# Kernel tuning notes

Measured on AMD Instinct MI355X. Metric: run time of the kernel, lower is better.

Reference implementation:

```python
import jax, jax.numpy as jnp
import numpy as np

N_NODES = 100000
N_EDGES = 1600000
IN_CH = 128
HID = 128   # 2 * out_channels
OUT_CH = 64


def setup_inputs() -> dict:
    key = jax.random.key(0)
    k1, k2, k3, k4, k5, k6 = jax.random.split(key, 6)
    x = jax.random.normal(k1, (N_NODES, IN_CH), dtype=jnp.float32)
    edge_index = jax.random.randint(k2, (2, N_EDGES), 0, N_NODES, dtype=jnp.int64)
    W1 = jax.random.normal(k3, (IN_CH, HID), dtype=jnp.float32) / np.sqrt(IN_CH)
    b1 = jax.random.normal(k4, (HID,), dtype=jnp.float32) * 0.01
    W2 = jax.random.normal(k5, (HID, OUT_CH), dtype=jnp.float32) / np.sqrt(HID)
    b2 = jax.random.normal(k6, (OUT_CH,), dtype=jnp.float32) * 0.01
    return {"x": x, "edge_index": edge_index, "W1": W1, "b1": b1, "W2": W2, "b2": b2}


def _gcn_layer(x, src, dst, norm, W, b, n_nodes):
    # GCNConv: linear transform, then normalized scatter-add aggregation + bias
    h = x @ W                                   # [N, d_out]
    msg = h[src] * norm[:, None]                # gather + edge normalize, [E+N, d_out]
    out = jax.ops.segment_sum(msg, dst, num_segments=n_nodes)
    return out + b


def reference(x, edge_index, W1, b1, W2, b2):
    n = x.shape[0]
    loop = jnp.arange(n, dtype=edge_index.dtype)
    # add self-loops (PyG GCNConv default)
    src = jnp.concatenate([edge_index[0], loop])
    dst = jnp.concatenate([edge_index[1], loop])
    # symmetric normalization deg^-1/2[src] * deg^-1/2[dst]
    deg = jax.ops.segment_sum(jnp.ones_like(dst, x.dtype), dst, num_segments=n)
    dinv = jnp.where(deg > 0, jax.lax.rsqrt(deg), 0.0)
    norm = dinv[src] * dinv[dst]

    h = jax.nn.relu(_gcn_layer(x, src, dst, norm, W1, b1, n))
    out = jax.nn.relu(_gcn_layer(h, src, dst, norm, W2, b2, n))
    return out
```

## Files before the change

### kernel.cpp

```cpp
#include <hip/hip_runtime.h>
#include <hip/hip_fp16.h>

typedef _Float16 f16x8 __attribute__((ext_vector_type(8)));
typedef float f32x4 __attribute__((ext_vector_type(4)));

#define BSH 9
#define BSZ 512
#define CAP 12288

__global__ __launch_bounds__(256) void passA(const int* __restrict__ ei,
                                             int* __restrict__ bcount, int E, int NB) {
  __shared__ int hist[256];
  int t = threadIdx.x;
  hist[t] = 0;
  __syncthreads();
  for (int e = blockIdx.x * 256 + t; e < E; e += gridDim.x * 256)
    atomicAdd(&hist[ei[E + e] >> BSH], 1);
  __syncthreads();
  if (t < NB && hist[t]) atomicAdd(&bcount[t], hist[t]);
}

__global__ __launch_bounds__(256) void scanB(const int* __restrict__ bcount,
                                             int* __restrict__ bstart,
                                             int* __restrict__ bfill, int NB, int E) {
  __shared__ int s[256];
  int t = threadIdx.x;
  int v = (t < NB) ? bcount[t] : 0;
  s[t] = v;
  __syncthreads();
  for (int off = 1; off < 256; off <<= 1) {
    int add = (t >= off) ? s[t - off] : 0;
    __syncthreads();
    s[t] += add;
    __syncthreads();
  }
  if (t < NB) {
    int ex = s[t] - v;
    bstart[t] = ex;
    bfill[t] = ex;
  }
  if (t == 0) bstart[NB] = E;
}

template <int NC, int NWC, bool IN_F16, bool SCALE>
__device__ __forceinline__ void gemm_mfma_body(
    const void* __restrict__ Xv, const float* __restrict__ W,
    const float* __restrict__ dinv, _Float16* __restrict__ G, int nrows, int bid,
    _Float16* Bs) {
  int t = threadIdx.x;
  {
    int n = t % NC;
    int kh = (t / NC) * (NC / 2);
    constexpr int NBLK = (NC / 2) / 8;
#pragma unroll
    for (int b = 0; b < NBLK; ++b) {
      f16x8 tmp;
#pragma unroll
      for (int j = 0; j < 8; ++j)
        tmp[j] = (_Float16)W[(size_t)(kh + b * 8 + j) * NC + n];
      *(f16x8*)(&Bs[n * 136 + kh + b * 8]) = tmp;
    }
  }
  __syncthreads();

  int w = t >> 6, lane = t & 63;
  int m = lane & 15, q = lane >> 4;
  int wr = (w / NWC) * 64, wc = (w % NWC) * 64;
  int row0 = bid * ((4 / NWC) * 64);

  f32x4 acc[4][4];
#pragma unroll
  for (int rt = 0; rt < 4; ++rt)
#pragma unroll
    for (int ct = 0; ct < 4; ++ct)
#pragma unroll
      for (int qq = 0; qq < 4; ++qq) acc[rt][ct][qq] = 0.f;

#pragma unroll
  for (int kc = 0; kc < 4; ++kc) {
    int kbase = kc * 32 + q * 8;
    f16x8 af[4];
#pragma unroll
    for (int rt = 0; rt < 4; ++rt) {
      int row = row0 + wr + rt * 16 + m;
      if constexpr (IN_F16) {
        f16x8 a = {0, 0, 0, 0, 0, 0, 0, 0};
        if (row < nrows) a = *(const f16x8*)((const _Float16*)Xv + (size_t)row * 128 + kbase);
        af[rt] = a;
      } else {
        float4 x0 = {0, 0, 0, 0}, x1 = {0, 0, 0, 0};
        if (row < nrows) {
          const float* Xf = (const float*)Xv;
          x0 = *(const float4*)(Xf + (size_t)row * 128 + kbase);
          x1 = *(const float4*)(Xf + (size_t)row * 128 + kbase + 4);
        }
        f16x8 a;
        a[0] = (_Float16)x0.x; a[1] = (_Float16)x0.y;
        a[2] = (_Float16)x0.z; a[3] = (_Float16)x0.w;
        a[4] = (_Float16)x1.x; a[5] = (_Float16)x1.y;
        a[6] = (_Float16)x1.z; a[7] = (_Float16)x1.w;
        af[rt] = a;
      }
    }
    f16x8 bf[4];
#pragma unroll
    for (int ct = 0; ct < 4; ++ct) {
      int n = wc + ct * 16 + m;
      bf[ct] = *(f16x8*)(&Bs[n * 136 + kbase]);
    }
#pragma unroll
    for (int rt = 0; rt < 4; ++rt)
#pragma unroll
      for (int ct = 0; ct < 4; ++ct)
        acc[rt][ct] = __builtin_amdgcn_mfma_f32_16x16x32_f16(af[rt], bf[ct],
                                                             acc[rt][ct], 0, 0, 0);
  }
#pragma unroll
  for (int rt = 0; rt < 4; ++rt) {
#pragma unroll
    for (int r = 0; r < 4; ++r) {
      int row = row0 + wr + rt * 16 + q * 4 + r;
      if (row < nrows) {
        float d = SCALE ? dinv[row] : 1.f;
#pragma unroll
        for (int ct = 0; ct < 4; ++ct) {
          int col = wc + ct * 16 + m;
          G[(size_t)row * NC + col] = (_Float16)(acc[rt][ct][r] * d);
        }
      }
    }
  }
}

__global__ __launch_bounds__(256) void fused_gemm_passB(
    const float* __restrict__ X, const float* __restrict__ W1,
    _Float16* __restrict__ G, int nrows, int GB,
    const int* __restrict__ ei, int* __restrict__ bfill,
    unsigned int* __restrict__ pairs, int E, int PB) {
  __shared__ char smem[128 * 136 * 2];
  int g = blockIdx.x;
  int M2 = 2 * (GB < PB ? GB : PB);
  bool is_gemm;
  int bid;
  if (g < M2) { is_gemm = (g & 1) == 0; bid = g >> 1; }
  else        { is_gemm = (GB > PB);    bid = g - M2 + (GB < PB ? GB : PB); }
  if (is_gemm) {
    gemm_mfma_body<128, 2, false, false>(X, W1, nullptr, G, nrows, bid,
                                         (_Float16*)smem);
  } else {
    int* hist = (int*)smem;
    int* gbase = (int*)(smem + 1024);
    int t = threadIdx.x;
    hist[t] = 0;
    __syncthreads();
    int d[8], s[8], lp[8], bb[8];
    int base = bid * 2048;
#pragma unroll
    for (int u = 0; u < 8; ++u) {
      int e = base + u * 256 + t;
      if (e < E) {
        d[u] = ei[E + e];
        s[u] = ei[e];
        bb[u] = d[u] >> BSH;
        lp[u] = atomicAdd(&hist[bb[u]], 1);
      } else {
        bb[u] = -1;
      }
    }
    __syncthreads();
    if (hist[t]) gbase[t] = atomicAdd(&bfill[t], hist[t]);
    __syncthreads();
#pragma unroll
    for (int u = 0; u < 8; ++u)
      if (bb[u] >= 0)
        pairs[gbase[bb[u]] + lp[u]] =
            ((unsigned int)(d[u] & (BSZ - 1)) << 17) | (unsigned int)s[u];
  }
}

__global__ __launch_bounds__(512) void passC(const unsigned int* __restrict__ pairs,
                                             const int* __restrict__ bstart,
                                             int* __restrict__ rowstart,
                                             int* __restrict__ deg,
                                             float* __restrict__ dinv,
                                             int* __restrict__ csr, int N) {
  __shared__ int hcnt[BSZ];
  __shared__ int lfill[BSZ];
  __shared__ int ss[512];
  __shared__ int lcsr[CAP];
  int b = blockIdx.x;
  int t = threadIdx.x;
  int lo = bstart[b], hi = bstart[b + 1];
  int cnt = hi - lo;
  int nbase = b << BSH;
  hcnt[t] = 0;
  __syncthreads();
  for (int k = lo + t; k < hi; k += 512)
    atomicAdd(&hcnt[(pairs[k] >> 17) & (BSZ - 1)], 1);
  __syncthreads();
  int v = hcnt[t];
  ss[t] = v;
  __syncthreads();
  for (int off = 1; off < 512; off <<= 1) {
    int add = (t >= off) ? ss[t - off] : 0;
    __syncthreads();
    ss[t] += add;
    __syncthreads();
  }
  int ex = ss[t] - v;
  lfill[t] = ex;
  int node = nbase + t;
  if (node < N) {
    rowstart[node] = lo + ex;
    deg[node] = v;
    dinv[node] = rsqrtf((float)(v + 1));
  }
  __syncthreads();
  bool fits = (cnt <= CAP);
  for (int k = lo + t; k < hi; k += 512) {
    unsigned int p = pairs[k];
    int pos = atomicAdd(&lfill[(p >> 17) & (BSZ - 1)], 1);
    int src = (int)(p & 0x1FFFFu);
    if (fits) lcsr[pos] = src;
    else      csr[lo + pos] = src;
  }
  __syncthreads();
  if (fits)
    for (int k = t; k < cnt; k += 512) csr[lo + k] = lcsr[k];
}

#define HPAD 144
__global__ __launch_bounds__(256) void agg128_mm(
    const __half* __restrict__ G, const int* __restrict__ csr,
    const int* __restrict__ rowstart, const int* __restrict__ deg,
    const float* __restrict__ dinv, const float* __restrict__ b1,
    const float* __restrict__ W2, _Float16* __restrict__ g2, int N) {
  __shared__ _Float16 Ws[64 * 136];
  __shared__ _Float16 Hs[4][16 * HPAD];
  int t = threadIdx.x;
  {
    int n = t & 63;
    int kh = (t >> 6) * 32;
#pragma unroll
    for (int b = 0; b < 4; ++b) {
      f16x8 tmp;
#pragma unroll
      for (int j = 0; j < 8; ++j)
        tmp[j] = (_Float16)W2[(size_t)(kh + b * 8 + j) * 64 + n];
      *(f16x8*)(&Ws[n * 136 + kh + b * 8]) = tmp;
    }
  }
  __syncthreads();

  int w = t >> 6, lane = t & 63;
  int m = lane & 15, q = lane >> 4;
  const __half2* Gp = (const __half2*)G;
  float2 bb = ((const float2*)b1)[lane];
  int node0 = (blockIdx.x * 4 + w) * 16;
  if (node0 >= N) return;

  _Float16* H = Hs[w];
#pragma unroll 1
  for (int u = 0; u < 16; ++u) {
    int i = node0 + u;
    float2 h = {0.f, 0.f};
    if (i < N) {
      int ii = __builtin_amdgcn_readfirstlane(i);
      float di = dinv[ii];
      float2 g = __half22float2(Gp[(size_t)ii * 64 + lane]);
      float2 a = {di * g.x, di * g.y};
      int s = rowstart[ii];
      int d = deg[ii];
      int k = 0;
      for (; k + 3 < d; k += 4) {
        int s0 = csr[s + k], s1 = csr[s + k + 1];
        int s2 = csr[s + k + 2], s3 = csr[s + k + 3];
        float w0 = dinv[s0], w1 = dinv[s1], w2 = dinv[s2], w3 = dinv[s3];
        float2 v0 = __half22float2(Gp[(size_t)s0 * 64 + lane]);
        float2 v1 = __half22float2(Gp[(size_t)s1 * 64 + lane]);
        float2 v2 = __half22float2(Gp[(size_t)s2 * 64 + lane]);
        float2 v3 = __half22float2(Gp[(size_t)s3 * 64 + lane]);
        a.x = fmaf(w0, v0.x, a.x); a.y = fmaf(w0, v0.y, a.y);
        a.x = fmaf(w1, v1.x, a.x); a.y = fmaf(w1, v1.y, a.y);
        a.x = fmaf(w2, v2.x, a.x); a.y = fmaf(w2, v2.y, a.y);
        a.x = fmaf(w3, v3.x, a.x); a.y = fmaf(w3, v3.y, a.y);
      }
      for (; k < d; ++k) {
        int s0 = csr[s + k];
        float w0 = dinv[s0];
        float2 v0 = __half22float2(Gp[(size_t)s0 * 64 + lane]);
        a.x = fmaf(w0, v0.x, a.x); a.y = fmaf(w0, v0.y, a.y);
      }
      h.x = fmaxf(fmaf(di, a.x, bb.x), 0.f);
      h.y = fmaxf(fmaf(di, a.y, bb.y), 0.f);
    }
    H[u * HPAD + 2 * lane]     = (_Float16)h.x;
    H[u * HPAD + 2 * lane + 1] = (_Float16)h.y;
  }

  f32x4 acc[4];
#pragma unroll
  for (int ct = 0; ct < 4; ++ct)
#pragma unroll
    for (int qq = 0; qq < 4; ++qq) acc[ct][qq] = 0.f;
#pragma unroll
  for (int kc = 0; kc < 4; ++kc) {
    int kb = kc * 32 + q * 8;
    f16x8 af = *(f16x8*)(&H[m * HPAD + kb]);
#pragma unroll
    for (int ct = 0; ct < 4; ++ct) {
      f16x8 bf = *(f16x8*)(&Ws[(ct * 16 + m) * 136 + kb]);
      acc[ct] = __builtin_amdgcn_mfma_f32_16x16x32_f16(af, bf, acc[ct], 0, 0, 0);
    }
  }
#pragma unroll
  for (int r = 0; r < 4; ++r) {
    int i = node0 + q * 4 + r;
    if (i < N) {
      float di = dinv[i];
#pragma unroll
      for (int ct = 0; ct < 4; ++ct)
        g2[(size_t)i * 64 + ct * 16 + m] = (_Float16)(acc[ct][r] * di);
    }
  }
}

__global__ __launch_bounds__(256) void agg64(
    const __half* __restrict__ G, const int* __restrict__ csr,
    const int* __restrict__ rowstart, const int* __restrict__ deg,
    const float* __restrict__ dinv, const float* __restrict__ bias,
    float* __restrict__ out, int n) {
  int wid = blockIdx.x * 4 + (threadIdx.x >> 6);
  if (wid >= n) return;
  int i = __builtin_amdgcn_readfirstlane(wid);
  int lane = threadIdx.x & 63;
  int e2 = lane >> 5, f = lane & 31;
  const __half2* Gp = (const __half2*)G;
  int r0 = rowstart[i];
  int d = deg[i];
  float2 acc = {0.f, 0.f};
  for (int k = 0; k < d; k += 4) {
    int kA = k + e2, kB = k + 2 + e2;
    int iA = i, iB = i;
    float wA = 0.f, wB = 0.f;
    if (kA < d) { iA = csr[r0 + kA]; wA = 1.f; }
    if (kB < d) { iB = csr[r0 + kB]; wB = 1.f; }
    float2 vA = __half22float2(Gp[(size_t)iA * 32 + f]);
    float2 vB = __half22float2(Gp[(size_t)iB * 32 + f]);
    acc.x = fmaf(wA, vA.x, acc.x); acc.y = fmaf(wA, vA.y, acc.y);
    acc.x = fmaf(wB, vB.x, acc.x); acc.y = fmaf(wB, vB.y, acc.y);
  }
  acc.x += __shfl_xor(acc.x, 32);
  acc.y += __shfl_xor(acc.y, 32);
  if (e2 == 0) {
    float di = dinv[i];
    float2 g = __half22float2(Gp[(size_t)i * 32 + f]);
    float2 b = ((const float2*)bias)[f];
    float2 o;
    o.x = fmaxf(fmaf(di, g.x + acc.x, b.x), 0.f);
    o.y = fmaxf(fmaf(di, g.y + acc.y, b.y), 0.f);
    ((float2*)out)[(size_t)i * 32 + f] = o;
  }
}

extern "C" void kernel_launch(void* const* d_in, const int* in_sizes, int n_in,
                              void* d_out, int out_size, void* d_ws, size_t ws_size,
                              hipStream_t stream) {
  const float* x  = (const float*)d_in[0];
  const int*   ei = (const int*)d_in[1];
  const float* W1 = (const float*)d_in[2];
  const float* b1 = (const float*)d_in[3];
  const float* W2 = (const float*)d_in[4];
  const float* b2 = (const float*)d_in[5];
  float* out = (float*)d_out;

  const int N = in_sizes[0] / 128;
  const int E = in_sizes[1] / 2;
  const int NB = (N + BSZ - 1) >> BSH;

  char* base = (char*)d_ws;
  size_t off = 0;
  auto alloc = [&](size_t bytes) -> void* {
    void* p = base + off;
    off += (bytes + 255) & ~(size_t)255;
    return p;
  };
  int*          bcount   = (int*)alloc(256 * 4);
  int*          bstart   = (int*)alloc(260 * 4);
  int*          bfill    = (int*)alloc(256 * 4);
  int*          deg      = (int*)alloc((size_t)N * 4);
  int*          rowstart = (int*)alloc((size_t)N * 4);
  float*        dinv     = (float*)alloc((size_t)N * 4);
  int*          csr      = (int*)alloc((size_t)E * 4);
  unsigned int* pairs    = (unsigned int*)alloc((size_t)E * 4);
  __half*       g1       = (__half*)alloc((size_t)N * 128 * 2);
  __half*       g2       = (__half*)alloc((size_t)N * 64 * 2);

  hipMemsetAsync(bcount, 0, 256 * 4, stream);
  passA<<<512, 256, 0, stream>>>(ei, bcount, E, NB);
  scanB<<<1, 256, 0, stream>>>(bcount, bstart, bfill, NB, E);

  int GB = (N + 127) / 128;
  int PB = (E + 2047) / 2048;
  fused_gemm_passB<<<GB + PB, 256, 0, stream>>>(x, W1, (_Float16*)g1, N, GB, ei,
                                                bfill, pairs, E, PB);
  passC<<<NB, 512, 0, stream>>>(pairs, bstart, rowstart, deg, dinv, csr, N);

  int nmm = (N + 63) / 64;
  agg128_mm<<<nmm, 256, 0, stream>>>(g1, csr, rowstart, deg, dinv, b1, W2,
                                     (_Float16*)g2, N);
  int ng = (N + 3) / 4;
  agg64<<<ng, 256, 0, stream>>>(g2, csr, rowstart, deg, dinv, b2, out, N);
}
```

Measured before the change: 342.4 us.

## Split fused layer-1 aggregation and layer-2 GEMM into separate kernels

```diff
diff --git a/kernel.cpp b/kernel.cpp
--- a/kernel.cpp
+++ b/kernel.cpp
@@ -229,14 +229,11 @@
     for (int k = t; k < cnt; k += 512) csr[lo + k] = lcsr[k];
 }
 
-#define HPAD 144
-__global__ __launch_bounds__(256) void agg128_mm(
-    const __half* __restrict__ G, const int* __restrict__ csr,
-    const int* __restrict__ rowstart, const int* __restrict__ deg,
-    const float* __restrict__ dinv, const float* __restrict__ b1,
-    const float* __restrict__ W2, _Float16* __restrict__ g2, int N) {
-  __shared__ _Float16 Ws[64 * 136];
-  __shared__ _Float16 Hs[4][16 * HPAD];
+__global__ __launch_bounds__(256) void gemm2s(const _Float16* __restrict__ X,
+                                              const float* __restrict__ W,
+                                              const float* __restrict__ dinv,
+                                              _Float16* __restrict__ G, int nrows) {
+  __shared__ _Float16 Bs[64 * 136];
   int t = threadIdx.x;
   {
     int n = t & 63;
@@ -246,83 +243,98 @@
       f16x8 tmp;
 #pragma unroll
       for (int j = 0; j < 8; ++j)
-        tmp[j] = (_Float16)W2[(size_t)(kh + b * 8 + j) * 64 + n];
-      *(f16x8*)(&Ws[n * 136 + kh + b * 8]) = tmp;
+        tmp[j] = (_Float16)W[(size_t)(kh + b * 8 + j) * 64 + n];
+      *(f16x8*)(&Bs[n * 136 + kh + b * 8]) = tmp;
     }
   }
   __syncthreads();
 
   int w = t >> 6, lane = t & 63;
   int m = lane & 15, q = lane >> 4;
-  const __half2* Gp = (const __half2*)G;
-  float2 bb = ((const float2*)b1)[lane];
-  int node0 = (blockIdx.x * 4 + w) * 16;
-  if (node0 >= N) return;
-
-  _Float16* H = Hs[w];
-#pragma unroll 1
-  for (int u = 0; u < 16; ++u) {
-    int i = node0 + u;
-    float2 h = {0.f, 0.f};
-    if (i < N) {
-      int ii = __builtin_amdgcn_readfirstlane(i);
-      float di = dinv[ii];
-      float2 g = __half22float2(Gp[(size_t)ii * 64 + lane]);
-      float2 a = {di * g.x, di * g.y};
-      int s = rowstart[ii];
-      int d = deg[ii];
-      int k = 0;
-      for (; k + 3 < d; k += 4) {
-        int s0 = csr[s + k], s1 = csr[s + k + 1];
-        int s2 = csr[s + k + 2], s3 = csr[s + k + 3];
-        float w0 = dinv[s0], w1 = dinv[s1], w2 = dinv[s2], w3 = dinv[s3];
-        float2 v0 = __half22float2(Gp[(size_t)s0 * 64 + lane]);
-        float2 v1 = __half22float2(Gp[(size_t)s1 * 64 + lane]);
-        float2 v2 = __half22float2(Gp[(size_t)s2 * 64 + lane]);
-        float2 v3 = __half22float2(Gp[(size_t)s3 * 64 + lane]);
-        a.x = fmaf(w0, v0.x, a.x); a.y = fmaf(w0, v0.y, a.y);
-        a.x = fmaf(w1, v1.x, a.x); a.y = fmaf(w1, v1.y, a.y);
-        a.x = fmaf(w2, v2.x, a.x); a.y = fmaf(w2, v2.y, a.y);
-        a.x = fmaf(w3, v3.x, a.x); a.y = fmaf(w3, v3.y, a.y);
-      }
-      for (; k < d; ++k) {
-        int s0 = csr[s + k];
-        float w0 = dinv[s0];
-        float2 v0 = __half22float2(Gp[(size_t)s0 * 64 + lane]);
-        a.x = fmaf(w0, v0.x, a.x); a.y = fmaf(w0, v0.y, a.y);
-      }
-      h.x = fmaxf(fmaf(di, a.x, bb.x), 0.f);
-      h.y = fmaxf(fmaf(di, a.y, bb.y), 0.f);
-    }
-    H[u * HPAD + 2 * lane]     = (_Float16)h.x;
-    H[u * HPAD + 2 * lane + 1] = (_Float16)h.y;
-  }
-
-  f32x4 acc[4];
-#pragma unroll
-  for (int ct = 0; ct < 4; ++ct)
-#pragma unroll
-    for (int qq = 0; qq < 4; ++qq) acc[ct][qq] = 0.f;
+  int row0 = blockIdx.x * 128 + w * 32;
+
+  f32x4 acc[2][4];
+#pragma unroll
+  for (int rt = 0; rt < 2; ++rt)
+#pragma unroll
+    for (int ct = 0; ct < 4; ++ct)
+#pragma unroll
+      for (int qq = 0; qq < 4; ++qq) acc[rt][ct][qq] = 0.f;
+
 #pragma unroll
   for (int kc = 0; kc < 4; ++kc) {
     int kb = kc * 32 + q * 8;
-    f16x8 af = *(f16x8*)(&H[m * HPAD + kb]);
+    f16x8 af[2];
+#pragma unroll
+    for (int rt = 0; rt < 2; ++rt) {
+      int row = row0 + rt * 16 + m;
+      f16x8 a = {0, 0, 0, 0, 0, 0, 0, 0};
+      if (row < nrows) a = *(const f16x8*)(X + (size_t)row * 128 + kb);
+      af[rt] = a;
+    }
 #pragma unroll
     for (int ct = 0; ct < 4; ++ct) {
-      f16x8 bf = *(f16x8*)(&Ws[(ct * 16 + m) * 136 + kb]);
-      acc[ct] = __builtin_amdgcn_mfma_f32_16x16x32_f16(af, bf, acc[ct], 0, 0, 0);
-    }
-  }
-#pragma unroll
-  for (int r = 0; r < 4; ++r) {
-    int i = node0 + q * 4 + r;
-    if (i < N) {
-      float di = dinv[i];
-#pragma unroll
-      for (int ct = 0; ct < 4; ++ct)
-        g2[(size_t)i * 64 + ct * 16 + m] = (_Float16)(acc[ct][r] * di);
-    }
-  }
+      f16x8 bf = *(f16x8*)(&Bs[(ct * 16 + m) * 136 + kb]);
+#pragma unroll
+      for (int rt = 0; rt < 2; ++rt)
+        acc[rt][ct] = __builtin_amdgcn_mfma_f32_16x16x32_f16(af[rt], bf,
+                                                             acc[rt][ct], 0, 0, 0);
+    }
+  }
+#pragma unroll
+  for (int rt = 0; rt < 2; ++rt) {
+#pragma unroll
+    for (int r = 0; r < 4; ++r) {
+      int row = row0 + rt * 16 + q * 4 + r;
+      if (row < nrows) {
+        float d = dinv[row];
+#pragma unroll
+        for (int ct = 0; ct < 4; ++ct)
+          G[(size_t)row * 64 + ct * 16 + m] = (_Float16)(acc[rt][ct][r] * d);
+      }
+    }
+  }
+}
+
+__global__ __launch_bounds__(256) void agg128(
+    const __half* __restrict__ G, const int* __restrict__ csr,
+    const int* __restrict__ rowstart, const int* __restrict__ deg,
+    const float* __restrict__ dinv, const float* __restrict__ bias,
+    __half* __restrict__ out, int n) {
+  int wid = blockIdx.x * 4 + (threadIdx.x >> 6);
+  if (wid >= n) return;
+  int i = __builtin_amdgcn_readfirstlane(wid);
+  int lane = threadIdx.x & 63;
+  const __half2* Gp = (const __half2*)G;
+  float di = dinv[i];
+  float2 g = __half22float2(Gp[(size_t)i * 64 + lane]);
+  float2 a = {di * g.x, di * g.y};
+  int s = rowstart[i];
+  int d = deg[i];
+  int k = 0;
+  for (; k + 3 < d; k += 4) {
+    int s0 = csr[s + k], s1 = csr[s + k + 1];
+    int s2 = csr[s + k + 2], s3 = csr[s + k + 3];
+    float w0 = dinv[s0], w1 = dinv[s1], w2 = dinv[s2], w3 = dinv[s3];
+    float2 v0 = __half22float2(Gp[(size_t)s0 * 64 + lane]);
+    float2 v1 = __half22float2(Gp[(size_t)s1 * 64 + lane]);
+    float2 v2 = __half22float2(Gp[(size_t)s2 * 64 + lane]);
+    float2 v3 = __half22float2(Gp[(size_t)s3 * 64 + lane]);
+    a.x = fmaf(w0, v0.x, a.x); a.y = fmaf(w0, v0.y, a.y);
+    a.x = fmaf(w1, v1.x, a.x); a.y = fmaf(w1, v1.y, a.y);
+    a.x = fmaf(w2, v2.x, a.x); a.y = fmaf(w2, v2.y, a.y);
+    a.x = fmaf(w3, v3.x, a.x); a.y = fmaf(w3, v3.y, a.y);
+  }
+  for (; k < d; ++k) {
+    int s0 = csr[s + k];
+    float w0 = dinv[s0];
+    float2 v0 = __half22float2(Gp[(size_t)s0 * 64 + lane]);
+    a.x = fmaf(w0, v0.x, a.x); a.y = fmaf(w0, v0.y, a.y);
+  }
+  float2 b = ((const float2*)bias)[lane];
+  float ox = fmaxf(fmaf(di, a.x, b.x), 0.f);
+  float oy = fmaxf(fmaf(di, a.y, b.y), 0.f);
+  ((__half2*)out)[(size_t)i * 64 + lane] = __floats2half2_rn(ox, oy);
 }
 
 __global__ __launch_bounds__(256) void agg64(
@@ -394,6 +406,7 @@
   int*          csr      = (int*)alloc((size_t)E * 4);
   unsigned int* pairs    = (unsigned int*)alloc((size_t)E * 4);
   __half*       g1       = (__half*)alloc((size_t)N * 128 * 2);
+  __half*       x2       = (__half*)alloc((size_t)N * 128 * 2);
   __half*       g2       = (__half*)alloc((size_t)N * 64 * 2);
 
   hipMemsetAsync(bcount, 0, 256 * 4, stream);
@@ -406,9 +419,10 @@
                                                 bfill, pairs, E, PB);
   passC<<<NB, 512, 0, stream>>>(pairs, bstart, rowstart, deg, dinv, csr, N);
 
-  int nmm = (N + 63) / 64;
-  agg128_mm<<<nmm, 256, 0, stream>>>(g1, csr, rowstart, deg, dinv, b1, W2,
-                                     (_Float16*)g2, N);
   int ng = (N + 3) / 4;
+  agg128<<<ng, 256, 0, stream>>>(g1, csr, rowstart, deg, dinv, b1, x2, N);
+  int G2B = (N + 127) / 128;
+  gemm2s<<<G2B, 256, 0, stream>>>((const _Float16*)x2, W2, dinv,
+                                  (_Float16*)g2, N);
   agg64<<<ng, 256, 0, stream>>>(g2, csr, rowstart, deg, dinv, b2, out, N);
 }
```

Measured after the change: 311.0 us. -9.2%, faster.
